# Kernel tuning notes

Hardware: AMD Instinct MI355X
Metric: run time of the kernel (lower is better)

## Reference

```python
import jax, jax.numpy as jnp
import numpy as np

N, C, K, H = 131072, 256, 32, 8      # points, dim, patch_size, heads
NW = N // K                           # number of windows (4096)
POS_BND = int(0.8 * K)                # 25, as in OctFormer RPE (dilation=1)
RPE_NUM = 2 * POS_BND + 1             # 51


def layer_norm(x, g, b, eps=1e-5):
    m = x.mean(-1, keepdims=True)
    v = jnp.var(x, axis=-1, keepdims=True)
    return (x - m) * jax.lax.rsqrt(v + eps) * g + b


def setup_inputs() -> dict:
    key = jax.random.key(0)
    ks = jax.random.split(key, 12)
    s = 0.02
    return dict(
        data=jax.random.normal(ks[0], (N, C), jnp.float32),
        nbr_idx=jax.random.randint(ks[1], (N, 27), 0, N, dtype=jnp.int32),
        rel_pos=(jax.random.randint(ks[2], (NW, K, K, 3), 0, 2 * K + 1, dtype=jnp.int32) - K),
        patch_mask=jnp.zeros((NW, K, K), jnp.float32),
        w_cpe=jax.random.normal(ks[3], (27, C), jnp.float32) * s,
        bn_g=jnp.ones((C,), jnp.float32), bn_b=jnp.zeros((C,), jnp.float32),
        n1_g=jnp.ones((C,), jnp.float32), n1_b=jnp.zeros((C,), jnp.float32),
        w_qkv=jax.random.normal(ks[4], (C, 3 * C), jnp.float32) * s,
        b_qkv=jnp.zeros((3 * C,), jnp.float32),
        w_proj=jax.random.normal(ks[5], (C, C), jnp.float32) * s,
        b_proj=jnp.zeros((C,), jnp.float32),
        rpe_table=jax.random.normal(ks[6], (3 * RPE_NUM, H), jnp.float32) * s,
        n2_g=jnp.ones((C,), jnp.float32), n2_b=jnp.zeros((C,), jnp.float32),
        w_fc1=jax.random.normal(ks[7], (C, 4 * C), jnp.float32) * s,
        b_fc1=jnp.zeros((4 * C,), jnp.float32),
        w_fc2=jax.random.normal(ks[8], (4 * C, C), jnp.float32) * s,
        b_fc2=jnp.zeros((C,), jnp.float32),
    )


def reference(data, nbr_idx, rel_pos, patch_mask, w_cpe, bn_g, bn_b,
              n1_g, n1_b, w_qkv, b_qkv, w_proj, b_proj, rpe_table,
              n2_g, n2_b, w_fc1, b_fc1, w_fc2, b_fc2):
    # CPE: depthwise 27-neighbor octree conv + eval-mode batchnorm affine
    cpe = jnp.einsum('njc,jc->nc', data[nbr_idx], w_cpe)  # [N,27,C] gather
    data = data + (cpe * bn_g + bn_b)
    # data_to_windows: [N,C] -> [NW,K,C] (N divisible by K)
    x = data.reshape(NW, K, C)

    # windowed attention with inline RPE + additive patch mask
    h = layer_norm(x, n1_g, n1_b)
    qkv = (h @ w_qkv + b_qkv).reshape(NW, K, 3, H, C // H)
    q, k, v = qkv[:, :, 0], qkv[:, :, 1], qkv[:, :, 2]
    scale = (C // H) ** -0.5
    attn = jnp.einsum('nqhd,nkhd->nhqk', q * scale, k)     # [NW,H,K,K]
    idx = jnp.clip(rel_pos, -POS_BND, POS_BND) + POS_BND + jnp.arange(3) * RPE_NUM
    rpe = rpe_table[idx].sum(3)                             # [NW,K,K,H]
    attn = attn + rpe.transpose(0, 3, 1, 2) + patch_mask[:, None]
    attn = jax.nn.softmax(attn, axis=-1)
    out = jnp.einsum('nhqk,nkhd->nqhd', attn, v).reshape(NW, K, C)
    x = x + (out @ w_proj + b_proj)                         # gamma1 = 1

    # MLP (GELU, exact erf like torch default)
    h2 = layer_norm(x, n2_g, n2_b)
    x = x + (jax.nn.gelu(h2 @ w_fc1 + b_fc1, approximate=False) @ w_fc2 + b_fc2)
    return x.reshape(N, C)
```

## Files before the change

kernel.cpp:

```cpp
#include <hip/hip_runtime.h>
#include <stdint.h>


static constexpr int NPT   = 131072;
static constexpr int CC    = 256;
static constexpr int NWIN  = 4096;
static constexpr int NHEAD = 8;

using u16 = unsigned short;
using u32 = unsigned int;
using u8  = unsigned char;

typedef __bf16 bf16x8 __attribute__((ext_vector_type(8)));
typedef float  f32x4  __attribute__((ext_vector_type(4)));
typedef u32    u32x4  __attribute__((ext_vector_type(4)));
typedef u32    u32x2  __attribute__((ext_vector_type(2)));

__device__ __forceinline__ float b2f(u16 u) {
  union { float f; u32 i; } v; v.i = ((u32)u) << 16; return v.f;
}
__device__ __forceinline__ u16 f2b(float f) {
  u32 x = __float_as_uint(f);
  return (u16)((x + 0x7fffu + ((x >> 16) & 1u)) >> 16);
}

__device__ __forceinline__ u8 f2fp8(float f) {
  const u32 s = (__float_as_uint(f) >> 24) & 0x80u;
  float a = fabsf(f);
  if (a >= 0.015625f) {
    u32 b = __float_as_uint(a);
    u32 rb = b + 0x7FFFFu + ((b >> 20) & 1u);
    u32 E = (rb >> 23) - 120u;
    return (u8)(s | (E << 3) | ((rb >> 20) & 7u));
  }
  int k = (int)rintf(a * 512.0f);
  return (u8)(s | (u32)k);
}

template <int J>
__device__ __forceinline__ float fp82f(u32 d) {
#if defined(__has_builtin)
#if __has_builtin(__builtin_amdgcn_cvt_f32_fp8)
  return __builtin_amdgcn_cvt_f32_fp8(d, J);
#else
  const u32 u = (d >> (8 * J)) & 0xFFu;
  const u32 e = (u >> 3) & 15u, m = u & 7u;
  float v = e ? __uint_as_float(((e + 120u) << 23) | (m << 20))
              : (float)m * 0.001953125f;
  return (u & 0x80u) ? -v : v;
#endif
#else
  const u32 u = (d >> (8 * J)) & 0xFFu;
  const u32 e = (u >> 3) & 15u, m = u & 7u;
  float v = e ? __uint_as_float(((e + 120u) << 23) | (m << 20))
              : (float)m * 0.001953125f;
  return (u & 0x80u) ? -v : v;
#endif
}

__device__ __forceinline__ void gload_lds16(const void* g, void* l) {
  using gptr_t = const __attribute__((address_space(1))) uint32_t*;
  using lptr_t = __attribute__((address_space(3))) uint32_t*;
  __builtin_amdgcn_global_load_lds((gptr_t)(uintptr_t)g,
                                   (lptr_t)(uint32_t)(uintptr_t)l, 16, 0, 0);
}

__global__ __launch_bounds__(256) void k_f2b8(const float* __restrict__ in,
                                              u8* __restrict__ out, int n4) {
  for (int i = blockIdx.x * 256 + threadIdx.x; i < n4; i += gridDim.x * 256) {
    float4 v = ((const float4*)in)[i];
    u32 o = (u32)f2fp8(v.x) | ((u32)f2fp8(v.y) << 8) |
            ((u32)f2fp8(v.z) << 16) | ((u32)f2fp8(v.w) << 24);
    ((u32*)out)[i] = o;
  }
}

__global__ __launch_bounds__(256) void k_transpose_f2b(const float* __restrict__ in,
                                                       u16* __restrict__ out, int R, int Cc) {
  int i = blockIdx.x * 256 + threadIdx.x;
  if (i >= R * Cc) return;
  int c = i / R, r = i - c * R;
  out[i] = f2b(in[r * Cc + c]);
}

__global__ __launch_bounds__(256) void k_cpe_ln1(
    const float* __restrict__ data, const int* __restrict__ nbr,
    const u8* __restrict__ datab, const float* __restrict__ w_cpe,
    const float* __restrict__ bn_g, const float* __restrict__ bn_b,
    const float* __restrict__ n1_g, const float* __restrict__ n1_b,
    float* __restrict__ xo, u16* __restrict__ ho) {
  const int wv   = threadIdx.x >> 6;
  const int lane = threadIdx.x & 63;
  const int n    = blockIdx.x * 4 + wv;
  const int c0   = lane * 4;

  int myidx = 0;
  if (lane < 27) myidx = nbr[n * 27 + lane];

  float a0 = 0.f, a1 = 0.f, a2 = 0.f, a3 = 0.f;
#pragma unroll
  for (int j = 0; j < 27; j++) {
    const int idx = __builtin_amdgcn_readlane(myidx, j);
    const u32 d = *(const u32*)(datab + (size_t)idx * CC + c0);
    const float4 wj = *(const float4*)(w_cpe + j * CC + c0);
    a0 += fp82f<0>(d) * wj.x;
    a1 += fp82f<1>(d) * wj.y;
    a2 += fp82f<2>(d) * wj.z;
    a3 += fp82f<3>(d) * wj.w;
  }

  const float4 dv = *(const float4*)(data + (size_t)n * CC + c0);
  const float4 g4 = *(const float4*)(bn_g + c0);
  const float4 b4 = *(const float4*)(bn_b + c0);
  float x0 = dv.x + a0 * g4.x + b4.x;
  float x1 = dv.y + a1 * g4.y + b4.y;
  float x2 = dv.z + a2 * g4.z + b4.z;
  float x3 = dv.w + a3 * g4.w + b4.w;
  *(float4*)(xo + (size_t)n * CC + c0) = make_float4(x0, x1, x2, x3);

  float s  = x0 + x1 + x2 + x3;
  float s2 = x0 * x0 + x1 * x1 + x2 * x2 + x3 * x3;
#pragma unroll
  for (int m = 1; m <= 32; m <<= 1) { s += __shfl_xor(s, m); s2 += __shfl_xor(s2, m); }
  const float mean = s * (1.f / 256.f);
  const float var  = s2 * (1.f / 256.f) - mean * mean;
  const float inv  = rsqrtf(var + 1e-5f);

  const float4 ng = *(const float4*)(n1_g + c0);
  const float4 nb4 = *(const float4*)(n1_b + c0);
  u32x2 o;
  o[0] = (u32)f2b((x0 - mean) * inv * ng.x + nb4.x) |
         ((u32)f2b((x1 - mean) * inv * ng.y + nb4.y) << 16);
  o[1] = (u32)f2b((x2 - mean) * inv * ng.z + nb4.z) |
         ((u32)f2b((x3 - mean) * inv * ng.w + nb4.w) << 16);
  *(u32x2*)(ho + (size_t)n * CC + c0) = o;
}

__global__ __launch_bounds__(256) void k_ln2(const float* __restrict__ x,
                                             const float* __restrict__ g,
                                             const float* __restrict__ b,
                                             u16* __restrict__ h) {
  const int row = blockIdx.x * 4 + (threadIdx.x >> 6);
  const int l = threadIdx.x & 63;
  const float4 xv = ((const float4*)(x + (size_t)row * CC))[l];
  float s  = xv.x + xv.y + xv.z + xv.w;
  float s2 = xv.x * xv.x + xv.y * xv.y + xv.z * xv.z + xv.w * xv.w;
#pragma unroll
  for (int m = 1; m <= 32; m <<= 1) { s += __shfl_xor(s, m); s2 += __shfl_xor(s2, m); }
  const float mean = s * (1.f / 256.f);
  const float var  = s2 * (1.f / 256.f) - mean * mean;
  const float inv  = rsqrtf(var + 1e-5f);
  const int c = l * 4;
  ushort4 o;
  o.x = f2b((xv.x - mean) * inv * g[c + 0] + b[c + 0]);
  o.y = f2b((xv.y - mean) * inv * g[c + 1] + b[c + 1]);
  o.z = f2b((xv.z - mean) * inv * g[c + 2] + b[c + 2]);
  o.w = f2b((xv.w - mean) * inv * g[c + 3] + b[c + 3]);
  ((ushort4*)(h + (size_t)row * CC))[l] = o;
}

template <int KD, int ND, int EPI>
__global__ __launch_bounds__(256) void k_gemm(const u16* __restrict__ A,
                                              const u16* __restrict__ Bt,
                                              const float* __restrict__ bias,
                                              u16* __restrict__ outb,
                                              float* __restrict__ outf) {
  __shared__ __align__(16) u16 As[128 * 64];
  __shared__ __align__(16) u16 Bs[128 * 64];
  const int tid = threadIdx.x;
  const int lane = tid & 63;
  const int wv = tid >> 6;
  const int wm = (wv >> 1) * 64;
  const int wn = (wv & 1) * 64;
  const int l15 = lane & 15;
  const int lhi = lane >> 4;
  const int m0 = blockIdx.y * 128;
  const int n0 = blockIdx.x * 128;

  f32x4 acc[4][4] = {};

  for (int k0 = 0; k0 < KD; k0 += 64) {
#pragma unroll
    for (int i = 0; i < 4; i++) {
      const int off = i * 4096 + tid * 16;
      const int row = off >> 7;
      const int ke  = (off & 127) >> 1;
      gload_lds16(A  + (size_t)(m0 + row) * KD + k0 + ke, (char*)As + off);
      gload_lds16(Bt + (size_t)(n0 + row) * KD + k0 + ke, (char*)Bs + off);
    }
    __syncthreads();
#pragma unroll
    for (int kk = 0; kk < 2; kk++) {
      bf16x8 fa[4], fb[4];
#pragma unroll
      for (int t = 0; t < 4; t++) {
        fa[t] = *(const bf16x8*)&As[(wm + t * 16 + l15) * 64 + kk * 32 + lhi * 8];
        fb[t] = *(const bf16x8*)&Bs[(wn + t * 16 + l15) * 64 + kk * 32 + lhi * 8];
      }
#pragma unroll
      for (int mi = 0; mi < 4; mi++)
#pragma unroll
        for (int ni = 0; ni < 4; ni++)
          acc[mi][ni] = __builtin_amdgcn_mfma_f32_16x16x32_bf16(fa[mi], fb[ni],
                                                                acc[mi][ni], 0, 0, 0);
    }
    __syncthreads();
  }

#pragma unroll
  for (int mi = 0; mi < 4; mi++) {
#pragma unroll
    for (int ni = 0; ni < 4; ni++) {
      const int col = n0 + wn + ni * 16 + l15;
      const float bc = bias[col];
#pragma unroll
      for (int r = 0; r < 4; r++) {
        const int row = m0 + wm + mi * 16 + lhi * 4 + r;
        const size_t o = (size_t)row * ND + col;
        float v = acc[mi][ni][r] + bc;
        if constexpr (EPI == 0) {
          outb[o] = f2b(v);
        } else if constexpr (EPI == 1) {
          outf[o] += v;
        } else {
          v = 0.5f * v * (1.0f + erff(v * 0.70710678118654752f));
          outb[o] = f2b(v);
        }
      }
    }
  }
}

__global__ __launch_bounds__(512, 4) void k_attn(const u16* __restrict__ qkv,
                                                 const int* __restrict__ rel_pos,
                                                 const float* __restrict__ pmask,
                                                 const float* __restrict__ rpet,
                                                 u16* __restrict__ out) {
  constexpr int HS = 1288;
  __shared__ __align__(16) u16 smem[24 * HS + 2448];
  u16* sQ = smem;
  u16* sK = smem + 8 * HS;
  u16* sV = smem + 16 * HS;
  float* sT = (float*)(smem + 24 * HS);

  const int tid = threadIdx.x;
  const int nw  = blockIdx.x;
  const int w32 = nw * 32;

  for (int i = tid; i < 1224; i += 512) {
    int h = i / 153, ix = i - h * 153;
    sT[i] = rpet[ix * 8 + h];
  }
#pragma unroll
  for (int j = 0; j < 4; j++) {
    int id  = j * 512 + tid;
    int mat = id >> 10;
    int id1 = id & 1023;
    int h = id1 >> 7, q = (id1 >> 2) & 31, s = id1 & 3;
    u32x4 v = *(const u32x4*)(qkv + (size_t)(w32 + q) * 768 + mat * 256 + h * 32 + s * 8);
    u16* dst = (mat ? sK : sQ) + h * HS + q * 40 + s * 8;
    *(u32x4*)dst = v;
  }
#pragma unroll
  for (int j = 0; j < 2; j++) {
    int id = j * 512 + tid;
    int p = id >> 5, dc = id & 31;
    u32x4 v = *(const u32x4*)(qkv + (size_t)(w32 + p) * 768 + 512 + dc * 8);
    const u16* pv = (const u16*)&v;
#pragma unroll
    for (int jj = 0; jj < 8; jj++) {
      int d = dc * 8 + jj;
      sV[(d >> 5) * HS + (d & 31) * 40 + p] = pv[jj];
    }
  }
  __syncthreads();

  const int h = tid >> 6;
  const int lane = tid & 63;
  const int g = lane >> 4, c = lane & 15;
  const f32x4 zero = {0.f, 0.f, 0.f, 0.f};

  bf16x8 fq[2], fk[2];
#pragma unroll
  for (int t = 0; t < 2; t++) {
    fq[t] = *(const bf16x8*)&sQ[h * HS + (t * 16 + c) * 40 + g * 8];
    fk[t] = *(const bf16x8*)&sK[h * HS + (t * 16 + c) * 40 + g * 8];
  }
  f32x4 S[2][2];
#pragma unroll
  for (int qt = 0; qt < 2; qt++)
#pragma unroll
    for (int kt = 0; kt < 2; kt++)
      S[qt][kt] = __builtin_amdgcn_mfma_f32_16x16x32_bf16(fq[qt], fk[kt], zero, 0, 0, 0);

  const float sc = 0.17677669529663687f;
#pragma unroll
  for (int qt = 0; qt < 2; qt++) {
#pragma unroll
    for (int r = 0; r < 4; r++) {
      const int q = qt * 16 + g * 4 + r;
      const int* rp = rel_pos + ((size_t)(w32 + q) * 32) * 3;
      const float* pm = pmask + (size_t)(w32 + q) * 32;
      float v[2];
#pragma unroll
      for (int kt = 0; kt < 2; kt++) {
        const int k = kt * 16 + c;
        int r0 = rp[k * 3], r1 = rp[k * 3 + 1], r2 = rp[k * 3 + 2];
        r0 = min(max(r0, -25), 25);
        r1 = min(max(r1, -25), 25);
        r2 = min(max(r2, -25), 25);
        const float b = sT[h * 153 + 25 + r0] + sT[h * 153 + 76 + r1] +
                        sT[h * 153 + 127 + r2] + pm[k];
        v[kt] = S[qt][kt][r] * sc + b;
      }
      float m = fmaxf(v[0], v[1]);
#pragma unroll
      for (int d = 1; d <= 8; d <<= 1) m = fmaxf(m, __shfl_xor(m, d));
      const float e0 = __expf(v[0] - m);
      const float e1 = __expf(v[1] - m);
      float ssum = e0 + e1;
#pragma unroll
      for (int d = 1; d <= 8; d <<= 1) ssum += __shfl_xor(ssum, d);
      const float inv = 1.0f / ssum;
      sQ[h * HS + q * 40 + c]      = f2b(e0 * inv);
      sQ[h * HS + q * 40 + 16 + c] = f2b(e1 * inv);
    }
  }
  __builtin_amdgcn_sched_barrier(0);

  bf16x8 fp[2], fv[2];
#pragma unroll
  for (int t = 0; t < 2; t++) {
    fp[t] = *(const bf16x8*)&sQ[h * HS + (t * 16 + c) * 40 + g * 8];
    fv[t] = *(const bf16x8*)&sV[h * HS + (t * 16 + c) * 40 + g * 8];
  }
  f32x4 OT[2][2];
#pragma unroll
  for (int dt = 0; dt < 2; dt++)
#pragma unroll
    for (int qt = 0; qt < 2; qt++)
      OT[dt][qt] = __builtin_amdgcn_mfma_f32_16x16x32_bf16(fv[dt], fp[qt], zero, 0, 0, 0);

  __syncthreads();
  u16* OL = sK;
#pragma unroll
  for (int dt = 0; dt < 2; dt++)
#pragma unroll
    for (int qt = 0; qt < 2; qt++)
#pragma unroll
      for (int r = 0; r < 4; r++) {
        const int d = dt * 16 + g * 4 + r, q = qt * 16 + c;
        OL[q * 264 + h * 32 + d] = f2b(OT[dt][qt][r]);
      }
  __syncthreads();

  {
    const int q = tid >> 4, ch = tid & 15;
    u32x4 w0 = *(const u32x4*)&OL[q * 264 + ch * 16];
    u32x4 w1 = *(const u32x4*)&OL[q * 264 + ch * 16 + 8];
    u16* ob = out + (size_t)(w32 + q) * 256 + ch * 16;
    *(u32x4*)ob = w0;
    *((u32x4*)ob + 1) = w1;
  }
}

extern "C" void kernel_launch(void* const* d_in, const int* in_sizes, int n_in,
                              void* d_out, int out_size, void* d_ws, size_t ws_size,
                              hipStream_t stream) {
  const float* data   = (const float*)d_in[0];
  const int*   nbr    = (const int*)d_in[1];
  const int*   relpos = (const int*)d_in[2];
  const float* pmask  = (const float*)d_in[3];
  const float* w_cpe  = (const float*)d_in[4];
  const float* bn_g   = (const float*)d_in[5];
  const float* bn_b   = (const float*)d_in[6];
  const float* n1_g   = (const float*)d_in[7];
  const float* n1_b   = (const float*)d_in[8];
  const float* w_qkv  = (const float*)d_in[9];
  const float* b_qkv  = (const float*)d_in[10];
  const float* w_proj = (const float*)d_in[11];
  const float* b_proj = (const float*)d_in[12];
  const float* rpet   = (const float*)d_in[13];
  const float* n2_g   = (const float*)d_in[14];
  const float* n2_b   = (const float*)d_in[15];
  const float* w_fc1  = (const float*)d_in[16];
  const float* b_fc1  = (const float*)d_in[17];
  const float* w_fc2  = (const float*)d_in[18];
  const float* b_fc2  = (const float*)d_in[19];
  float* xout = (float*)d_out;

  char* pw = (char*)d_ws;
  u16* buf1 = (u16*)pw; pw += (size_t)NPT * 1024 * 2;
  u16* buf2 = (u16*)pw; pw += (size_t)NPT * 256 * 2;
  u16* wqkvT = (u16*)pw; pw += 768 * 256 * 2;
  u16* wprojT = (u16*)pw; pw += 256 * 256 * 2;
  u16* wfc1T = (u16*)pw; pw += 1024 * 256 * 2;
  u16* wfc2T = (u16*)pw; pw += 256 * 1024 * 2;
  u8* data8 = (u8*)buf1;

  k_f2b8<<<2048, 256, 0, stream>>>(data, data8, NPT * 256 / 4);
  k_transpose_f2b<<<(256 * 768 + 255) / 256, 256, 0, stream>>>(w_qkv, wqkvT, 256, 768);
  k_transpose_f2b<<<(256 * 256 + 255) / 256, 256, 0, stream>>>(w_proj, wprojT, 256, 256);
  k_transpose_f2b<<<(256 * 1024 + 255) / 256, 256, 0, stream>>>(w_fc1, wfc1T, 256, 1024);
  k_transpose_f2b<<<(1024 * 256 + 255) / 256, 256, 0, stream>>>(w_fc2, wfc2T, 1024, 256);

  k_cpe_ln1<<<NPT / 4, 256, 0, stream>>>(data, nbr, data8, w_cpe, bn_g, bn_b, n1_g, n1_b,
                                         xout, buf2);
  k_gemm<256, 768, 0><<<dim3(6, 1024), 256, 0, stream>>>(buf2, wqkvT, b_qkv, buf1, nullptr);
  k_attn<<<NWIN, 512, 0, stream>>>(buf1, relpos, pmask, rpet, buf2);
  k_gemm<256, 256, 1><<<dim3(2, 1024), 256, 0, stream>>>(buf2, wprojT, b_proj, nullptr, xout);
  k_ln2<<<NPT / 4, 256, 0, stream>>>(xout, n2_g, n2_b, buf2);
  k_gemm<256, 1024, 2><<<dim3(8, 1024), 256, 0, stream>>>(buf2, wfc1T, b_fc1, buf1, nullptr);
  k_gemm<1024, 256, 1><<<dim3(2, 1024), 256, 0, stream>>>(buf1, wfc2T, b_fc2, nullptr, xout);
}
```

Measured before the change: 956.9 us.

## Fuse proj GEMM with LN2, batch CPE gathers, swizzle GEMM blocks, merge weight prep

The separate projection GEMM and LayerNorm-2 kernels become one kernel. Each block computes a full 256-wide row tile, adds bias and the residual, then writes both the fp32 residual and the normalized bf16 activations. This removes one full read and write pass over the activations. The CPE kernel now issues all 27 neighbour gathers before accumulating, to expose more memory-level parallelism at the cost of extra registers. The generic GEMM remaps block indices with a group-of-8 swizzle for cache locality, and the four weight-transpose launches are merged into one.

```diff
diff --git a/kernel.cpp b/kernel.cpp
--- a/kernel.cpp
+++ b/kernel.cpp
@@ -75,12 +75,21 @@
   }
 }
 
-__global__ __launch_bounds__(256) void k_transpose_f2b(const float* __restrict__ in,
-                                                       u16* __restrict__ out, int R, int Cc) {
+__global__ __launch_bounds__(256) void k_prep_w(
+    const float* __restrict__ wqkv, const float* __restrict__ wproj,
+    const float* __restrict__ wfc1, const float* __restrict__ wfc2,
+    u16* __restrict__ oqkv, u16* __restrict__ oproj,
+    u16* __restrict__ ofc1, u16* __restrict__ ofc2) {
   int i = blockIdx.x * 256 + threadIdx.x;
-  if (i >= R * Cc) return;
-  int c = i / R, r = i - c * R;
-  out[i] = f2b(in[r * Cc + c]);
+  if (i < 196608) {
+    int c = i >> 8, r = i & 255; oqkv[i] = f2b(wqkv[r * 768 + c]);
+  } else if (i < 262144) {
+    i -= 196608; int c = i >> 8, r = i & 255; oproj[i] = f2b(wproj[r * 256 + c]);
+  } else if (i < 524288) {
+    i -= 262144; int c = i >> 8, r = i & 255; ofc1[i] = f2b(wfc1[r * 1024 + c]);
+  } else {
+    i -= 524288; int c = i >> 10, r = i & 1023; ofc2[i] = f2b(wfc2[r * 256 + c]);
+  }
 }
 
 __global__ __launch_bounds__(256) void k_cpe_ln1(
@@ -97,16 +106,21 @@
   int myidx = 0;
   if (lane < 27) myidx = nbr[n * 27 + lane];
 
-  float a0 = 0.f, a1 = 0.f, a2 = 0.f, a3 = 0.f;
+  u32 d[27];
 #pragma unroll
   for (int j = 0; j < 27; j++) {
     const int idx = __builtin_amdgcn_readlane(myidx, j);
-    const u32 d = *(const u32*)(datab + (size_t)idx * CC + c0);
+    d[j] = *(const u32*)(datab + (size_t)idx * CC + c0);
+  }
+
+  float a0 = 0.f, a1 = 0.f, a2 = 0.f, a3 = 0.f;
+#pragma unroll
+  for (int j = 0; j < 27; j++) {
     const float4 wj = *(const float4*)(w_cpe + j * CC + c0);
-    a0 += fp82f<0>(d) * wj.x;
-    a1 += fp82f<1>(d) * wj.y;
-    a2 += fp82f<2>(d) * wj.z;
-    a3 += fp82f<3>(d) * wj.w;
+    a0 += fp82f<0>(d[j]) * wj.x;
+    a1 += fp82f<1>(d[j]) * wj.y;
+    a2 += fp82f<2>(d[j]) * wj.z;
+    a3 += fp82f<3>(d[j]) * wj.w;
   }
 
   const float4 dv = *(const float4*)(data + (size_t)n * CC + c0);
@@ -134,29 +148,6 @@
   o[1] = (u32)f2b((x2 - mean) * inv * ng.z + nb4.z) |
          ((u32)f2b((x3 - mean) * inv * ng.w + nb4.w) << 16);
   *(u32x2*)(ho + (size_t)n * CC + c0) = o;
-}
-
-__global__ __launch_bounds__(256) void k_ln2(const float* __restrict__ x,
-                                             const float* __restrict__ g,
-                                             const float* __restrict__ b,
-                                             u16* __restrict__ h) {
-  const int row = blockIdx.x * 4 + (threadIdx.x >> 6);
-  const int l = threadIdx.x & 63;
-  const float4 xv = ((const float4*)(x + (size_t)row * CC))[l];
-  float s  = xv.x + xv.y + xv.z + xv.w;
-  float s2 = xv.x * xv.x + xv.y * xv.y + xv.z * xv.z + xv.w * xv.w;
-#pragma unroll
-  for (int m = 1; m <= 32; m <<= 1) { s += __shfl_xor(s, m); s2 += __shfl_xor(s2, m); }
-  const float mean = s * (1.f / 256.f);
-  const float var  = s2 * (1.f / 256.f) - mean * mean;
-  const float inv  = rsqrtf(var + 1e-5f);
-  const int c = l * 4;
-  ushort4 o;
-  o.x = f2b((xv.x - mean) * inv * g[c + 0] + b[c + 0]);
-  o.y = f2b((xv.y - mean) * inv * g[c + 1] + b[c + 1]);
-  o.z = f2b((xv.z - mean) * inv * g[c + 2] + b[c + 2]);
-  o.w = f2b((xv.w - mean) * inv * g[c + 3] + b[c + 3]);
-  ((ushort4*)(h + (size_t)row * CC))[l] = o;
 }
 
 template <int KD, int ND, int EPI>
@@ -174,8 +165,13 @@
   const int wn = (wv & 1) * 64;
   const int l15 = lane & 15;
   const int lhi = lane >> 4;
-  const int m0 = blockIdx.y * 128;
-  const int n0 = blockIdx.x * 128;
+
+  const int gx = gridDim.x;
+  const int bid = blockIdx.y * gx + blockIdx.x;
+  const int cpx = (gx * gridDim.y) >> 3;
+  const int swz = (bid & 7) * cpx + (bid >> 3);
+  const int m0 = (swz / gx) * 128;
+  const int n0 = (swz % gx) * 128;
 
   f32x4 acc[4][4] = {};
 
@@ -226,6 +222,83 @@
           v = 0.5f * v * (1.0f + erff(v * 0.70710678118654752f));
           outb[o] = f2b(v);
         }
+      }
+    }
+  }
+}
+
+__global__ __launch_bounds__(256) void k_proj_ln2(
+    const u16* __restrict__ A, const u16* __restrict__ Bt,
+    const float* __restrict__ bias, float* __restrict__ xo,
+    const float* __restrict__ n2g, const float* __restrict__ n2b,
+    u16* __restrict__ h2) {
+  __shared__ __align__(16) u16 As[128 * 64];
+  __shared__ __align__(16) u16 Bs[256 * 64];
+  const int tid = threadIdx.x;
+  const int lane = tid & 63;
+  const int wv = tid >> 6;
+  const int l15 = lane & 15;
+  const int g = lane >> 4;
+  const int m0 = blockIdx.x * 128;
+  const int wm = wv * 32;
+
+  f32x4 acc[2][16] = {};
+
+  for (int k0 = 0; k0 < 256; k0 += 64) {
+#pragma unroll
+    for (int i = 0; i < 4; i++) {
+      const int off = i * 4096 + tid * 16;
+      const int row = off >> 7, ke = (off & 127) >> 1;
+      gload_lds16(A + (size_t)(m0 + row) * 256 + k0 + ke, (char*)As + off);
+    }
+#pragma unroll
+    for (int i = 0; i < 8; i++) {
+      const int off = i * 4096 + tid * 16;
+      const int row = off >> 7, ke = (off & 127) >> 1;
+      gload_lds16(Bt + (size_t)row * 256 + k0 + ke, (char*)Bs + off);
+    }
+    __syncthreads();
+#pragma unroll
+    for (int kk = 0; kk < 2; kk++) {
+      bf16x8 fa[2];
+#pragma unroll
+      for (int t = 0; t < 2; t++)
+        fa[t] = *(const bf16x8*)&As[(wm + t * 16 + l15) * 64 + kk * 32 + g * 8];
+#pragma unroll
+      for (int ni = 0; ni < 16; ni++) {
+        bf16x8 fb = *(const bf16x8*)&Bs[(ni * 16 + l15) * 64 + kk * 32 + g * 8];
+#pragma unroll
+        for (int mi = 0; mi < 2; mi++)
+          acc[mi][ni] = __builtin_amdgcn_mfma_f32_16x16x32_bf16(fa[mi], fb,
+                                                                acc[mi][ni], 0, 0, 0);
+      }
+    }
+    __syncthreads();
+  }
+
+#pragma unroll
+  for (int mi = 0; mi < 2; mi++) {
+#pragma unroll
+    for (int r = 0; r < 4; r++) {
+      const int row = m0 + wm + mi * 16 + g * 4 + r;
+      float v[16];
+      float s = 0.f, s2 = 0.f;
+#pragma unroll
+      for (int ni = 0; ni < 16; ni++) {
+        const int col = ni * 16 + l15;
+        float t = acc[mi][ni][r] + bias[col] + xo[(size_t)row * 256 + col];
+        v[ni] = t; s += t; s2 += t * t;
+      }
+#pragma unroll
+      for (int m = 1; m <= 8; m <<= 1) { s += __shfl_xor(s, m); s2 += __shfl_xor(s2, m); }
+      const float mean = s * (1.f / 256.f);
+      const float var  = s2 * (1.f / 256.f) - mean * mean;
+      const float inv  = rsqrtf(var + 1e-5f);
+#pragma unroll
+      for (int ni = 0; ni < 16; ni++) {
+        const int col = ni * 16 + l15;
+        xo[(size_t)row * 256 + col] = v[ni];
+        h2[(size_t)row * 256 + col] = f2b((v[ni] - mean) * inv * n2g[col] + n2b[col]);
       }
     }
   }
@@ -399,17 +472,14 @@
   u8* data8 = (u8*)buf1;
 
   k_f2b8<<<2048, 256, 0, stream>>>(data, data8, NPT * 256 / 4);
-  k_transpose_f2b<<<(256 * 768 + 255) / 256, 256, 0, stream>>>(w_qkv, wqkvT, 256, 768);
-  k_transpose_f2b<<<(256 * 256 + 255) / 256, 256, 0, stream>>>(w_proj, wprojT, 256, 256);
-  k_transpose_f2b<<<(256 * 1024 + 255) / 256, 256, 0, stream>>>(w_fc1, wfc1T, 256, 1024);
-  k_transpose_f2b<<<(1024 * 256 + 255) / 256, 256, 0, stream>>>(w_fc2, wfc2T, 1024, 256);
+  k_prep_w<<<3072, 256, 0, stream>>>(w_qkv, w_proj, w_fc1, w_fc2,
+                                     wqkvT, wprojT, wfc1T, wfc2T);
 
   k_cpe_ln1<<<NPT / 4, 256, 0, stream>>>(data, nbr, data8, w_cpe, bn_g, bn_b, n1_g, n1_b,
                                          xout, buf2);
   k_gemm<256, 768, 0><<<dim3(6, 1024), 256, 0, stream>>>(buf2, wqkvT, b_qkv, buf1, nullptr);
   k_attn<<<NWIN, 512, 0, stream>>>(buf1, relpos, pmask, rpet, buf2);
-  k_gemm<256, 256, 1><<<dim3(2, 1024), 256, 0, stream>>>(buf2, wprojT, b_proj, nullptr, xout);
-  k_ln2<<<NPT / 4, 256, 0, stream>>>(xout, n2_g, n2_b, buf2);
+  k_proj_ln2<<<1024, 256, 0, stream>>>(buf2, wprojT, b_proj, xout, n2_g, n2_b, buf2);
   k_gemm<256, 1024, 2><<<dim3(8, 1024), 256, 0, stream>>>(buf2, wfc1T, b_fc1, buf1, nullptr);
   k_gemm<1024, 256, 1><<<dim3(2, 1024), 256, 0, stream>>>(buf1, wfc2T, b_fc2, nullptr, xout);
 }
```

Result: faster. 916.3 us (-4.2%).
